# Kernel tuning notes

Measured on AMD Instinct MI355X. Metric: run time of the kernel, lower is better.

Reference implementation:

```python
import jax, jax.numpy as jnp
import numpy as np

M_GROUPS = 512  # fixed number of segments (== fill_max for ii)


def setup_inputs() -> dict:
    key = jax.random.key(0)
    ks = jax.random.split(key, 8)
    B, N, D = 4, 16384, 384
    x = jax.random.normal(ks[0], (B, N, D), dtype=jnp.float32)
    ii = jax.random.randint(ks[1], (N,), 0, M_GROUPS)
    s = 1.0 / np.sqrt(D)
    f_w = jax.random.uniform(ks[2], (D, D), jnp.float32, -s, s)
    f_b = jax.random.uniform(ks[3], (D,), jnp.float32, -s, s)
    g_w = jax.random.uniform(ks[4], (D, D), jnp.float32, -s, s)
    g_b = jax.random.uniform(ks[5], (D,), jnp.float32, -s, s)
    h_w = jax.random.uniform(ks[6], (D, D), jnp.float32, -s, s)
    h_b = jax.random.uniform(ks[7], (D,), jnp.float32, -s, s)
    return {"x": x, "ii": ii, "f_w": f_w, "f_b": f_b,
            "g_w": g_w, "g_b": g_b, "h_w": h_w, "h_b": h_b}


def reference(x, ii, f_w, f_b, g_w, g_b, h_w, h_b):
    # x: [B, N, D], ii: [N] group indices in [0, M_GROUPS)
    logits = x @ g_w.T + g_b                      # g(x): [B, N, D]
    exp_logits = jnp.exp(logits)
    # segment sum over n for each group m (== one-hot einsum 'bnm,bnd->bmd')
    seg = lambda e: jax.ops.segment_sum(e, ii, num_segments=M_GROUPS)
    sum_exp = jax.vmap(seg)(exp_logits)           # [B, M, D]
    denom = sum_exp[:, ii]                        # gather back: [B, N, D]
    w = exp_logits / (denom + 1e-6)
    fx = x @ f_w.T + f_b                          # f(x): [B, N, D]
    y = jax.vmap(seg)(fx * w)                     # [B, M, D]
    y = y @ h_w.T + h_b                           # h(y)
    return y[:, ii]                               # expand: [B, N, D]
```

## Files before the change

### kernel.cpp

```cpp
#include <hip/hip_runtime.h>
#include <hip/hip_bf16.h>

#define D 384
#define NROWS 16384
#define BATCH 4
#define MG 512
#define RTOT (BATCH * NROWS)
#define NC (2 * D)
#define JB 64
#define NJB (D / JB)
#define NKT 12

typedef __attribute__((ext_vector_type(8))) short bf16x8;
typedef __attribute__((ext_vector_type(4))) float f32x4;

static __device__ __forceinline__ unsigned short f2bf(float f) {
  unsigned int u = __float_as_uint(f);
  unsigned int r = u + 0x7fffu + ((u >> 16) & 1u);
  return (unsigned short)(r >> 16);
}
static __device__ __forceinline__ unsigned int cvtpk(float lo, float hi) {
  unsigned int r;
  asm("v_cvt_pk_bf16_f32 %0, %1, %2" : "=v"(r) : "v"(lo), "v"(hi));
  return r;
}
static __device__ __forceinline__ float frcp(float f) {
  float r;
  asm("v_rcp_f32 %0, %1" : "=v"(r) : "v"(f));
  return r;
}

typedef __attribute__((address_space(1))) const void gvoid_t;
typedef __attribute__((address_space(3))) void lvoid_t;
static __device__ __forceinline__ void gl16(const void* g, void* l) {
  __builtin_amdgcn_global_load_lds((gvoid_t*)g, (lvoid_t*)l, 16, 0, 0);
}

__global__ __launch_bounds__(512) void k_prep(
    const int* __restrict__ ii, const float* __restrict__ g_w,
    const float* __restrict__ f_w, const float* __restrict__ h_w,
    unsigned short* __restrict__ wt2, unsigned short* __restrict__ hw,
    int* __restrict__ csr_rows, int* __restrict__ grp_sorted,
    float* __restrict__ s12) {
  __shared__ int cnt[MG];
  __shared__ int scan[MG];
  const int blk = blockIdx.x;
  const int t = threadIdx.x;
  if (blk == 0) {
    cnt[t] = 0;
    __syncthreads();
    for (int n = t; n < NROWS; n += MG) atomicAdd(&cnt[ii[n]], 1);
    __syncthreads();
    const int v = cnt[t];
    scan[t] = v;
    __syncthreads();
#pragma unroll
    for (int o = 1; o < MG; o <<= 1) {
      int u = (t >= o) ? scan[t - o] : 0;
      __syncthreads();
      scan[t] += u;
      __syncthreads();
    }
    cnt[t] = scan[t] - v;
    __syncthreads();
    for (int n = t; n < NROWS; n += MG) {
      int m = ii[n];
      int pos = atomicAdd(&cnt[m], 1);
      csr_rows[pos] = n;
      grp_sorted[pos] = m;
    }
  } else if (blk < 64) {
    const int tot4 = 2 * BATCH * MG * D / 4;
    float4 z = {0.f, 0.f, 0.f, 0.f};
    for (int i = (blk - 1) * 512 + t; i < tot4; i += 63 * 512) ((float4*)s12)[i] = z;
  } else {
    const int tid0 = (blk - 64) * 512 + t;
    const int stride = 64 * 512;
    for (int idx = tid0; idx < NC * D; idx += stride) {
      int jblk = idx / (128 * D);
      int rem = idx % (128 * D);
      int c = rem / D, k = rem % D;
      int j = jblk * JB + (c & 63);
      float v = (c < JB) ? g_w[j * D + k] : f_w[j * D + k];
      wt2[idx] = f2bf(v);
    }
    for (int idx = tid0; idx < D * D; idx += stride) hw[idx] = f2bf(h_w[idx]);
  }
}

__global__ __launch_bounds__(512, 1) void k_gemm1(
    const float* __restrict__ x, const unsigned short* __restrict__ wt2,
    const float* __restrict__ g_b, const float* __restrict__ f_b,
    const int* __restrict__ csr_rows, const int* __restrict__ grp_sorted,
    float* __restrict__ s1acc, float* __restrict__ s2acc) {
  __shared__ __attribute__((aligned(16))) unsigned short As[NKT * 4096];
  __shared__ __attribute__((aligned(16))) unsigned short Bs[2][2][4096];
  __shared__ int grpS[128];

  const int tid = threadIdx.x;
  const int lane = tid & 63, wid = tid >> 6;
  const int wr = wid >> 2;
  const int wq = wid & 3;
  const int p = wq >> 1;
  const int u = wq & 1;
  const int blk = blockIdx.x;
  const int b = blk >> 7;
  const int ibl = (blk & 127) * 128;

  if (tid < 128) grpS[tid] = grp_sorted[ibl + tid];

  const int skb = ((lane & 3) ^ ((lane >> 3) & 3)) * 16;
  const int swz16 = ((lane >> 4) ^ ((lane >> 1) & 3)) * 16;

  const char* wtb = (const char*)wt2;
  const int prow = wid * 16 + (lane >> 2);
  const size_t bsrcoff = (size_t)prow * (D * 2) + skb;
  char* const bdstw = (char*)&Bs[0][0][0];
  gl16(wtb + 0 * (128 * D * 2) + bsrcoff, bdstw + wid * 1024);
  gl16(wtb + 1 * (128 * D * 2) + bsrcoff, bdstw + 8192 + wid * 1024);

  {
    const int arow = tid >> 2;
    const int grow = csr_rows[ibl + arow];
    const float* asrc = x + ((size_t)((b << 14) + grow)) * D + (tid & 3) * 8;
    const int aslot = (tid & 3) ^ ((tid >> 3) & 3);
    char* adst = (char*)As + arow * 64 + aslot * 16;
#pragma unroll
    for (int kt = 0; kt < NKT; ++kt) {
      const float4 v0 = *(const float4*)(asrc + kt * 32);
      const float4 v1 = *(const float4*)(asrc + kt * 32 + 4);
      int4 o;
      o.x = cvtpk(v0.x, v0.y);
      o.y = cvtpk(v0.z, v0.w);
      o.z = cvtpk(v1.x, v1.y);
      o.w = cvtpk(v1.z, v1.w);
      *(int4*)(adst + kt * 8192) = o;
    }
  }
  __syncthreads();

  f32x4 acc[4][4];
#pragma unroll
  for (int m = 0; m < 4; m++)
#pragma unroll
    for (int n = 0; n < 4; n++) acc[m][n] = (f32x4){0.f, 0.f, 0.f, 0.f};

#pragma unroll 1
  for (int e = 0; e < 3; ++e) {
#pragma unroll
    for (int kt = 0; kt < NKT; ++kt) {
      asm volatile("s_waitcnt vmcnt(0)\ns_barrier" ::: "memory");
      if (!(e == 2 && kt == 11)) {
        const int kt2 = (kt == 11) ? 0 : kt + 1;
        const int jbn = (kt == 11) ? 2 * e + 2 : 2 * e;
        char* nd = (char*)&Bs[(kt + 1) & 1][0][0] + wid * 1024;
        gl16(wtb + (size_t)jbn * (128 * D * 2) + kt2 * 64 + bsrcoff, nd);
        gl16(wtb + (size_t)(jbn + 1) * (128 * D * 2) + kt2 * 64 + bsrcoff, nd + 8192);
      }
      bf16x8 af[4], bfv[4];
      const char* ab = (const char*)As + kt * 8192;
#pragma unroll
      for (int m = 0; m < 4; m++)
        af[m] = *(const bf16x8*)(ab + (wr * 64 + m * 16 + (lane & 15)) * 64 + swz16);
      const char* bb = (const char*)&Bs[kt & 1][p][0];
#pragma unroll
      for (int n = 0; n < 4; n++) {
        const int c = (n < 2) ? (u * 32 + n * 16) : (64 + u * 32 + (n - 2) * 16);
        bfv[n] = *(const bf16x8*)(bb + (c + (lane & 15)) * 64 + swz16);
      }
      __builtin_amdgcn_s_setprio(1);
#pragma unroll
      for (int m = 0; m < 4; m++)
#pragma unroll
        for (int n = 0; n < 4; n++)
          acc[m][n] = __builtin_amdgcn_mfma_f32_16x16x32_bf16(af[m], bfv[n], acc[m][n], 0, 0, 0);
      __builtin_amdgcn_s_setprio(0);
    }

    {
      const int j0 = (2 * e + p) * JB;
      const int jA = j0 + u * 32 + (lane & 15);
      const float gb0 = g_b[jA], gb1 = g_b[jA + 16];
      const float fb0 = f_b[jA], fb1 = f_b[jA + 16];
      const int rowbase = wr * 64;

      int gmr[4][4];
#pragma unroll
      for (int m = 0; m < 4; m++)
#pragma unroll
        for (int r = 0; r < 4; r++)
          gmr[m][r] = grpS[rowbase + m * 16 + (lane >> 4) * 4 + r];

#pragma unroll
      for (int m = 0; m < 4; m++)
#pragma unroll
        for (int r = 0; r < 4; r++) {
          const float e0 = expf(acc[m][0][r] + gb0);
          const float e1 = expf(acc[m][1][r] + gb1);
          const float f0 = acc[m][2][r] + fb0;
          const float f1 = acc[m][3][r] + fb1;
          acc[m][0][r] = e0; acc[m][1][r] = e1;
          acc[m][2][r] = f0 * e0; acc[m][3][r] = f1 * e1;
        }

      const int gLo = grpS[rowbase], gHi = grpS[rowbase + 63];
      for (int g = gLo; g <= gHi; ++g) {
        float v0 = 0.f, v1 = 0.f, v2 = 0.f, v3 = 0.f;
#pragma unroll
        for (int m = 0; m < 4; m++)
#pragma unroll
          for (int r = 0; r < 4; r++)
            if (gmr[m][r] == g) {
              v0 += acc[m][0][r]; v1 += acc[m][1][r];
              v2 += acc[m][2][r]; v3 += acc[m][3][r];
            }
        v0 += __shfl_xor(v0, 16); v0 += __shfl_xor(v0, 32);
        v1 += __shfl_xor(v1, 16); v1 += __shfl_xor(v1, 32);
        v2 += __shfl_xor(v2, 16); v2 += __shfl_xor(v2, 32);
        v3 += __shfl_xor(v3, 16); v3 += __shfl_xor(v3, 32);
        if (lane < 16) {
          float* s1p = s1acc + ((size_t)(b * MG + g)) * D + j0 + u * 32 + lane;
          float* s2p = s2acc + ((size_t)(b * MG + g)) * D + j0 + u * 32 + lane;
          atomicAdd(s1p, v0);
          atomicAdd(s1p + 16, v1);
          atomicAdd(s2p, v2);
          atomicAdd(s2p + 16, v3);
        }
      }
    }
#pragma unroll
    for (int m = 0; m < 4; m++)
#pragma unroll
      for (int n = 0; n < 4; n++) acc[m][n] = (f32x4){0.f, 0.f, 0.f, 0.f};
  }
}

__global__ __launch_bounds__(256) void k_gemm2(
    const float* __restrict__ s1, const float* __restrict__ s2,
    const unsigned short* __restrict__ hw, const float* __restrict__ h_b,
    float* __restrict__ outpre) {
  const int tid = threadIdx.x, lane = tid & 63, wid = tid >> 6;
  const int r0 = blockIdx.y * 16;
  const int c0 = blockIdx.x * 64 + wid * 16;
  f32x4 acc = (f32x4){0.f, 0.f, 0.f, 0.f};
  const int arow = r0 + (lane & 15);
  const float* s1p = s1 + (size_t)arow * D + (lane >> 4) * 8;
  const float* s2p = s2 + (size_t)arow * D + (lane >> 4) * 8;
  const unsigned short* bRow = hw + (size_t)(c0 + (lane & 15)) * D + (lane >> 4) * 8;
#pragma unroll
  for (int kt = 0; kt < D / 32; kt++) {
    float4 u0 = *(const float4*)(s1p + kt * 32);
    float4 u1 = *(const float4*)(s1p + kt * 32 + 4);
    float4 w0 = *(const float4*)(s2p + kt * 32);
    float4 w1 = *(const float4*)(s2p + kt * 32 + 4);
    int4 yi;
    yi.x = cvtpk(w0.x * frcp(u0.x + 1e-6f), w0.y * frcp(u0.y + 1e-6f));
    yi.y = cvtpk(w0.z * frcp(u0.z + 1e-6f), w0.w * frcp(u0.w + 1e-6f));
    yi.z = cvtpk(w1.x * frcp(u1.x + 1e-6f), w1.y * frcp(u1.y + 1e-6f));
    yi.w = cvtpk(w1.z * frcp(u1.z + 1e-6f), w1.w * frcp(u1.w + 1e-6f));
    bf16x8 af = *(bf16x8*)&yi;
    bf16x8 bf_ = *(const bf16x8*)(bRow + kt * 32);
    acc = __builtin_amdgcn_mfma_f32_16x16x32_bf16(af, bf_, acc, 0, 0, 0);
  }
  const int col = c0 + (lane & 15);
  const float hb = h_b[col];
#pragma unroll
  for (int r = 0; r < 4; r++) {
    const int row = r0 + (lane >> 4) * 4 + r;
    outpre[(size_t)row * D + col] = acc[r] + hb;
  }
}

__global__ void k_gather(const float* __restrict__ outpre, const int* __restrict__ ii,
                         float* __restrict__ out) {
  const long total4 = (long)RTOT * (D / 4);
  for (long i = blockIdx.x * (long)blockDim.x + threadIdx.x; i < total4;
       i += (long)gridDim.x * blockDim.x) {
    const long row = i / (D / 4);
    const int q = (int)(i % (D / 4));
    const int b = (int)(row >> 14);
    const int n = (int)(row & (NROWS - 1));
    const int g = ii[n];
    ((float4*)out)[i] = ((const float4*)outpre)[((size_t)(b * MG + g)) * (D / 4) + q];
  }
}

extern "C" void kernel_launch(void* const* d_in, const int* in_sizes, int n_in,
                              void* d_out, int out_size, void* d_ws, size_t ws_size,
                              hipStream_t stream) {
  const float* x = (const float*)d_in[0];
  const int* ii = (const int*)d_in[1];
  const float* f_w = (const float*)d_in[2];
  const float* f_b = (const float*)d_in[3];
  const float* g_w = (const float*)d_in[4];
  const float* g_b = (const float*)d_in[5];
  const float* h_w = (const float*)d_in[6];
  const float* h_b = (const float*)d_in[7];
  float* out = (float*)d_out;

  char* ws = (char*)d_ws;
  size_t off = 0;
  auto alloc = [&](size_t bytes) {
    size_t p = off;
    off = (off + bytes + 255) & ~(size_t)255;
    return p;
  };
  unsigned short* wt2 = (unsigned short*)(ws + alloc((size_t)NC * D * 2));
  unsigned short* hw = (unsigned short*)(ws + alloc((size_t)D * D * 2));
  float* s1acc = (float*)(ws + alloc((size_t)BATCH * MG * D * 4));
  float* s2acc = (float*)(ws + alloc((size_t)BATCH * MG * D * 4));
  float* outpre = (float*)(ws + alloc((size_t)BATCH * MG * D * 4));
  int* csr_rows = (int*)(ws + alloc((size_t)NROWS * 4));
  int* grp_sorted = (int*)(ws + alloc((size_t)NROWS * 4));

  k_prep<<<dim3(128), dim3(512), 0, stream>>>(ii, g_w, f_w, h_w, wt2, hw, csr_rows,
                                              grp_sorted, s1acc);
  k_gemm1<<<dim3(512), dim3(512), 0, stream>>>(x, wt2, g_b, f_b, csr_rows, grp_sorted,
                                               s1acc, s2acc);
  k_gemm2<<<dim3(D / 64, (BATCH * MG) / 16), dim3(256), 0, stream>>>(s1acc, s2acc, hw, h_b,
                                                                     outpre);
  k_gather<<<dim3(4096), dim3(256), 0, stream>>>(outpre, ii, out);
}
```

Baseline: 150.3 us.

## Load GEMM1 B fragments directly from global into registers, drop LDS staging

The weight tile in k_gemm1 was previously staged into a double-buffered LDS array with global_load_lds and a barrier on every k-step. It is now read straight from global (L2-resident) into registers with a two-deep register prefetch, and the per-k barriers are removed. Launch bounds now allow two blocks per CU, since LDS use shrinks. The risk is more global/L2 traffic, because each wave fetches its own B fragments, plus uncoalesced 16-byte reads and higher register pressure under the tighter occupancy bound.

```diff
diff --git a/kernel.cpp b/kernel.cpp
--- a/kernel.cpp
+++ b/kernel.cpp
@@ -28,12 +28,6 @@
   float r;
   asm("v_rcp_f32 %0, %1" : "=v"(r) : "v"(f));
   return r;
-}
-
-typedef __attribute__((address_space(1))) const void gvoid_t;
-typedef __attribute__((address_space(3))) void lvoid_t;
-static __device__ __forceinline__ void gl16(const void* g, void* l) {
-  __builtin_amdgcn_global_load_lds((gvoid_t*)g, (lvoid_t*)l, 16, 0, 0);
 }
 
 __global__ __launch_bounds__(512) void k_prep(
@@ -88,36 +82,50 @@
   }
 }
 
-__global__ __launch_bounds__(512, 1) void k_gemm1(
+__global__ __launch_bounds__(512, 2) void k_gemm1(
     const float* __restrict__ x, const unsigned short* __restrict__ wt2,
     const float* __restrict__ g_b, const float* __restrict__ f_b,
     const int* __restrict__ csr_rows, const int* __restrict__ grp_sorted,
     float* __restrict__ s1acc, float* __restrict__ s2acc) {
   __shared__ __attribute__((aligned(16))) unsigned short As[NKT * 4096];
-  __shared__ __attribute__((aligned(16))) unsigned short Bs[2][2][4096];
   __shared__ int grpS[128];
 
   const int tid = threadIdx.x;
   const int lane = tid & 63, wid = tid >> 6;
   const int wr = wid >> 2;
-  const int wq = wid & 3;
-  const int p = wq >> 1;
-  const int u = wq & 1;
+  const int p = (wid >> 1) & 1;
+  const int u = wid & 1;
   const int blk = blockIdx.x;
   const int b = blk >> 7;
   const int ibl = (blk & 127) * 128;
 
   if (tid < 128) grpS[tid] = grp_sorted[ibl + tid];
 
-  const int skb = ((lane & 3) ^ ((lane >> 3) & 3)) * 16;
   const int swz16 = ((lane >> 4) ^ ((lane >> 1) & 3)) * 16;
 
-  const char* wtb = (const char*)wt2;
-  const int prow = wid * 16 + (lane >> 2);
-  const size_t bsrcoff = (size_t)prow * (D * 2) + skb;
-  char* const bdstw = (char*)&Bs[0][0][0];
-  gl16(wtb + 0 * (128 * D * 2) + bsrcoff, bdstw + wid * 1024);
-  gl16(wtb + 1 * (128 * D * 2) + bsrcoff, bdstw + 8192 + wid * 1024);
+  const unsigned short* bP[4];
+#pragma unroll
+  for (int n = 0; n < 4; n++) {
+    const int c = (n < 2) ? (u * 32 + n * 16) : (64 + u * 32 + (n - 2) * 16);
+    bP[n] = wt2 + (size_t)(c + (lane & 15)) * D + (lane >> 4) * 8;
+  }
+
+  bf16x8 b0[4], b1[4];
+
+#define LOADB(Bv, jb_, kt_)                                                    \
+  _Pragma("unroll") for (int n = 0; n < 4; n++) Bv[n] =                        \
+      *(const bf16x8*)(bP[n] + (size_t)(jb_) * (128 * D) + (kt_) * 32);
+
+#define STEPK(kt_, Bv)                                                         \
+  _Pragma("unroll") for (int m = 0; m < 4; m++) {                              \
+    const bf16x8 af = *(const bf16x8*)((const char*)As + (kt_) * 8192 +        \
+        (wr * 64 + m * 16 + (lane & 15)) * 64 + swz16);                        \
+    _Pragma("unroll") for (int n = 0; n < 4; n++)                              \
+      acc[m][n] =                                                              \
+          __builtin_amdgcn_mfma_f32_16x16x32_bf16(af, Bv[n], acc[m][n], 0, 0, 0); \
+  }
+
+  LOADB(b0, p, 0)
 
   {
     const int arow = tid >> 2;
@@ -147,38 +155,22 @@
 
 #pragma unroll 1
   for (int e = 0; e < 3; ++e) {
-#pragma unroll
-    for (int kt = 0; kt < NKT; ++kt) {
-      asm volatile("s_waitcnt vmcnt(0)\ns_barrier" ::: "memory");
-      if (!(e == 2 && kt == 11)) {
-        const int kt2 = (kt == 11) ? 0 : kt + 1;
-        const int jbn = (kt == 11) ? 2 * e + 2 : 2 * e;
-        char* nd = (char*)&Bs[(kt + 1) & 1][0][0] + wid * 1024;
-        gl16(wtb + (size_t)jbn * (128 * D * 2) + kt2 * 64 + bsrcoff, nd);
-        gl16(wtb + (size_t)(jbn + 1) * (128 * D * 2) + kt2 * 64 + bsrcoff, nd + 8192);
+    const int jb = 2 * e + p;
+#pragma unroll
+    for (int k2 = 0; k2 < 6; ++k2) {
+      const int kt = 2 * k2;
+      LOADB(b1, jb, kt + 1)
+      STEPK(kt, b0)
+      if (kt + 2 < NKT) {
+        LOADB(b0, jb, kt + 2)
+      } else if (e < 2) {
+        LOADB(b0, jb + 2, 0)
       }
-      bf16x8 af[4], bfv[4];
-      const char* ab = (const char*)As + kt * 8192;
-#pragma unroll
-      for (int m = 0; m < 4; m++)
-        af[m] = *(const bf16x8*)(ab + (wr * 64 + m * 16 + (lane & 15)) * 64 + swz16);
-      const char* bb = (const char*)&Bs[kt & 1][p][0];
-#pragma unroll
-      for (int n = 0; n < 4; n++) {
-        const int c = (n < 2) ? (u * 32 + n * 16) : (64 + u * 32 + (n - 2) * 16);
-        bfv[n] = *(const bf16x8*)(bb + (c + (lane & 15)) * 64 + swz16);
-      }
-      __builtin_amdgcn_s_setprio(1);
-#pragma unroll
-      for (int m = 0; m < 4; m++)
-#pragma unroll
-        for (int n = 0; n < 4; n++)
-          acc[m][n] = __builtin_amdgcn_mfma_f32_16x16x32_bf16(af[m], bfv[n], acc[m][n], 0, 0, 0);
-      __builtin_amdgcn_s_setprio(0);
+      STEPK(kt + 1, b1)
     }
 
     {
-      const int j0 = (2 * e + p) * JB;
+      const int j0 = jb * JB;
       const int jA = j0 + u * 32 + (lane & 15);
       const float gb0 = g_b[jA], gb1 = g_b[jA + 16];
       const float fb0 = f_b[jA], fb1 = f_b[jA + 16];
@@ -233,6 +225,8 @@
 #pragma unroll
       for (int n = 0; n < 4; n++) acc[m][n] = (f32x4){0.f, 0.f, 0.f, 0.f};
   }
+#undef LOADB
+#undef STEPK
 }
 
 __global__ __launch_bounds__(256) void k_gemm2(
```

Result: slower. 221.4 us (+47.2%).
